# Optimization experiments

Measured on AMD Instinct MI355X. Metric: run time of the kernel, lower is better.

## Reference

```python
import jax, jax.numpy as jnp
import numpy as np

B, S, D = 2, 2048, 2048
VOCAB = 32000
CUTOFFS = [1000, 2000, 5000, VOCAB]  # torch appends vocab_size
N_CLUSTERS = 3
HEAD_SIZE = CUTOFFS[0] + N_CLUSTERS  # 1003
LN_EPS = 1e-5
INIT = 0.02


def setup_inputs() -> dict:
    key = jax.random.key(0)
    ks = jax.random.split(key, 10)
    inp = {
        "x": jax.random.normal(ks[0], (B, S, D), dtype=jnp.float32),
        "targets": jax.random.randint(ks[1], (B, S), 0, VOCAB, dtype=jnp.int32),
        "gamma": jnp.ones((D,), jnp.float32),
        "beta": jnp.zeros((D,), jnp.float32),
        "head_w": jax.random.normal(ks[2], (HEAD_SIZE, D), jnp.float32) * INIT,
    }
    # tail clusters: hsz = D // 4**i, osz = cutoffs[i] - cutoffs[i-1]
    for i in range(1, 4):
        hsz = D // (4 ** i)
        osz = CUTOFFS[i] - CUTOFFS[i - 1]
        inp[f"t{i}_w1"] = jax.random.normal(ks[2 + 2 * i], (hsz, D), jnp.float32) * INIT
        inp[f"t{i}_w2"] = jax.random.normal(ks[3 + 2 * i], (osz, hsz), jnp.float32) * INIT
    return inp


def reference(x, targets, gamma, beta, head_w, t1_w1, t1_w2, t2_w1, t2_w2, t3_w1, t3_w2):
    # LayerNorm over last dim
    mu = jnp.mean(x, axis=-1, keepdims=True)
    var = jnp.mean(jnp.square(x - mu), axis=-1, keepdims=True)
    xn = (x - mu) * jax.lax.rsqrt(var + LN_EPS) * gamma + beta

    # shift: predict token t+1 from hidden t
    h = xn[:, :-1, :].reshape(-1, x.shape[-1])      # [N, D]
    lbl = targets[:, 1:].reshape(-1)                # [N]
    n = h.shape[0]
    rows = jnp.arange(n)

    # head: shortlist (first cutoff) + one logit per tail cluster
    head_lp = jax.nn.log_softmax(h @ head_w.T, axis=-1)  # [N, 1003]
    out = head_lp[rows, jnp.clip(lbl, 0, CUTOFFS[0] - 1)]

    tails = [(t1_w1, t1_w2), (t2_w1, t2_w2), (t3_w1, t3_w2)]
    for i, (w1, w2) in enumerate(tails):
        low, high = CUTOFFS[i], CUTOFFS[i + 1]
        tail_lp = jax.nn.log_softmax((h @ w1.T) @ w2.T, axis=-1)  # [N, osz]
        rel = jnp.clip(lbl - low, 0, high - low - 1)
        lp = head_lp[:, CUTOFFS[0] + i] + tail_lp[rows, rel]
        out = jnp.where((lbl >= low) & (lbl < high), lp, out)

    return -jnp.mean(out)  # NLL loss, matches .loss of AdaptiveLogSoftmaxWithLoss
```

## Files before the change

### kernel.cpp

```cpp
#include <hip/hip_runtime.h>
#include <hip/hip_bf16.h>
#include <math.h>

#define BB 2
#define SS 2048
#define DD 2048
#define NR (BB*(SS-1))
#define NRP 4096
#define MC_LD 1792
#define MT_LD 768
#define MT_P2 512
#define MT_P3 640

#define L2E 1.4426950408889634f
#define LSE_SHIFT 4.0f
#define LSE_NC (-LSE_SHIFT * L2E)
#define WSCALE 16.0f
#define WINV   0.0625f

typedef short  bh8   __attribute__((ext_vector_type(8)));
typedef float  f32x4 __attribute__((ext_vector_type(4)));
typedef long   l64x2 __attribute__((ext_vector_type(2)));

__device__ inline float bfl(unsigned short b) { return __uint_as_float(((unsigned)b) << 16); }
__device__ inline float expsh(float v) { return __builtin_amdgcn_exp2f(fmaf(v, L2E, LSE_NC)); }

__device__ inline float block_sum256(float v) {
    __shared__ float tmp[4];
    #pragma unroll
    for (int o = 32; o > 0; o >>= 1) v += __shfl_down(v, o, 64);
    int lane = threadIdx.x & 63, w = threadIdx.x >> 6;
    if (lane == 0) tmp[w] = v;
    __syncthreads();
    float r = tmp[0] + tmp[1] + tmp[2] + tmp[3];
    __syncthreads();
    return r;
}

__device__ inline unsigned pack_fp8x4(float a, float b, float c, float d) {
    unsigned r = 0;
    r = __builtin_amdgcn_cvt_pk_fp8_f32(a, b, r, false);
    r = __builtin_amdgcn_cvt_pk_fp8_f32(c, d, r, true);
    return r;
}

struct CastSegs {
    const float* src[7];
    void* dst[7];
    int n_src[7];
    int n_tot[7];
    int b0[7];
    int isfp8[7];
};
struct AParams {
    const float* x; const float* gamma; const float* beta;
    unsigned char* h8;
    CastSegs sg; int castBlocks;
    const int* targets;
    int *relH, *rel1, *rel2, *rel3;
    float *S1, *S2, *out;
};

__global__ __launch_bounds__(256) void stageA(AParams p) {
    int blk = blockIdx.x, tid = threadIdx.x;
    if (blk < NRP) {
        int n = blk;
        unsigned char* hr = p.h8 + (size_t)n * DD;
        if (n >= NR) { *(uint2*)(hr + tid * 8) = make_uint2(0,0); return; }
        int b = n / (SS - 1), t = n % (SS - 1);
        const float4* xr = (const float4*)(p.x + (size_t)(b * SS + t) * DD);
        float4 a = xr[tid * 2];
        float4 c = xr[tid * 2 + 1];
        float sum = a.x + a.y + a.z + a.w + c.x + c.y + c.z + c.w;
        sum = block_sum256(sum);
        float mu = sum * (1.0f / DD);
        float d[8] = {a.x-mu, a.y-mu, a.z-mu, a.w-mu, c.x-mu, c.y-mu, c.z-mu, c.w-mu};
        float sq = 0.f;
        #pragma unroll
        for (int i = 0; i < 8; ++i) sq += d[i] * d[i];
        sq = block_sum256(sq);
        float rstd = rsqrtf(sq * (1.0f / DD) + 1e-5f);
        const float4* g4 = (const float4*)p.gamma;
        const float4* be4 = (const float4*)p.beta;
        float4 g1 = g4[tid*2], g2 = g4[tid*2+1];
        float4 b1 = be4[tid*2], b2 = be4[tid*2+1];
        float gg[8] = {g1.x,g1.y,g1.z,g1.w,g2.x,g2.y,g2.z,g2.w};
        float bb[8] = {b1.x,b1.y,b1.z,b1.w,b2.x,b2.y,b2.z,b2.w};
        float o[8];
        #pragma unroll
        for (int i = 0; i < 8; ++i) o[i] = d[i] * rstd * gg[i] + bb[i];
        uint2 pk;
        pk.x = pack_fp8x4(o[0], o[1], o[2], o[3]);
        pk.y = pack_fp8x4(o[4], o[5], o[6], o[7]);
        *(uint2*)(hr + tid * 8) = pk;
        return;
    }
    blk -= NRP;
    if (blk < p.castBlocks) {
        int k = 0;
        #pragma unroll
        for (int i = 1; i < 7; ++i) if (blk >= p.sg.b0[i]) k = i;
        int i4 = (blk - p.sg.b0[k]) * 1024 + tid * 4;
        if (i4 >= p.sg.n_tot[k]) return;
        float4 v = make_float4(0.f,0.f,0.f,0.f);
        if (i4 < p.sg.n_src[k]) v = *(const float4*)(p.sg.src[k] + i4);
        if (p.sg.isfp8[k]) {
            unsigned pk = pack_fp8x4(v.x * WSCALE, v.y * WSCALE, v.z * WSCALE, v.w * WSCALE);
            *(unsigned*)((unsigned char*)p.sg.dst[k] + i4) = pk;
        } else {
            __align__(8) __hip_bfloat16 o[4] = {
                __float2bfloat16(v.x), __float2bfloat16(v.y),
                __float2bfloat16(v.z), __float2bfloat16(v.w)};
            *(uint2*)((__hip_bfloat16*)p.sg.dst[k] + i4) = *(uint2*)o;
        }
        return;
    }
    blk -= p.castBlocks;
    int n = blk * 256 + tid;
    if (n >= NRP) return;
    int lbl = -1;
    if (n < NR) {
        int b = n / (SS - 1), t = n % (SS - 1);
        lbl = p.targets[b * SS + t + 1];
    }
    bool v = n < NR;
    p.relH[n] = v ? (lbl < 1000 ? lbl : 999) : -1;
    int r1 = lbl - 1000;  p.rel1[n] = v ? (r1 < 0 ? 0 : (r1 > 999   ? 999   : r1)) : -1;
    int r2 = lbl - 2000;  p.rel2[n] = v ? (r2 < 0 ? 0 : (r2 > 2999  ? 2999  : r2)) : -1;
    int r3 = lbl - 5000;  p.rel3[n] = v ? (r3 < 0 ? 0 : (r3 > 26999 ? 26999 : r3)) : -1;
    p.S1[n] = 0.f; p.S2[n] = 0.f;
    if (n == 0) p.out[0] = 0.f;
}

__global__ __launch_bounds__(256) void mega_sk(
        const unsigned char* __restrict__ A,
        const unsigned char* __restrict__ W,
        __hip_bfloat16* __restrict__ P) {
    __shared__ __align__(16) unsigned char As[128 * 64];
    __shared__ __align__(16) unsigned char Ws[128 * 64];
    int tid = threadIdx.x, wv = tid >> 6, lane = tid & 63;
    int row0 = blockIdx.y * 128, col0 = blockIdx.x * 128;
    int kb = blockIdx.z * 1024, ke = kb + 1024;
    int wrow = (wv >> 1) * 64, wcol = (wv & 1) * 64;
    f32x4 acc[4][4];
    #pragma unroll
    for (int i = 0; i < 4; ++i)
        #pragma unroll
        for (int j = 0; j < 4; ++j) acc[i][j] = (f32x4){0.f,0.f,0.f,0.f};
    int sr = lane >> 2;
    int kp = (lane & 3) * 16;
    int mrow = lane & 15;
    int q16 = (lane >> 4) * 16;

    for (int k0 = kb; k0 < ke; k0 += 64) {
        __syncthreads();
        #pragma unroll
        for (int i = 0; i < 2; ++i) {
            int chunk = wv * 2 + i;
            int r = chunk * 16 + sr;
            const void* ga = A + (size_t)(row0 + r) * DD + k0 + kp;
            const void* gw = W + (size_t)(col0 + r) * DD + k0 + kp;
            void* la = (char*)As + chunk * 1024 + lane * 16;
            void* lw = (char*)Ws + chunk * 1024 + lane * 16;
            __builtin_amdgcn_global_load_lds(
                (const __attribute__((address_space(1))) void*)ga,
                (__attribute__((address_space(3))) void*)la, 16, 0, 0);
            __builtin_amdgcn_global_load_lds(
                (const __attribute__((address_space(1))) void*)gw,
                (__attribute__((address_space(3))) void*)lw, 16, 0, 0);
        }
        __syncthreads();
        l64x2 af[4], bfr[4];
        #pragma unroll
        for (int t = 0; t < 4; ++t) {
            af[t]  = *(const l64x2*)(As + (wrow + t*16 + mrow) * 64 + q16);
            bfr[t] = *(const l64x2*)(Ws + (wcol + t*16 + mrow) * 64 + q16);
        }
        #pragma unroll
        for (int s = 0; s < 2; ++s)
            #pragma unroll
            for (int i = 0; i < 4; ++i)
                #pragma unroll
                for (int j = 0; j < 4; ++j)
                    acc[i][j] = __builtin_amdgcn_mfma_f32_16x16x32_fp8_fp8(
                        af[i][s], bfr[j][s], acc[i][j], 0, 0, 0);
    }
    __hip_bfloat16* Cz = P + (size_t)blockIdx.z * NRP * MC_LD;
    int ccol = lane & 15, crow = (lane >> 4) * 4;
    #pragma unroll
    for (int i = 0; i < 4; ++i) {
        size_t gr0 = row0 + wrow + i*16 + crow;
        #pragma unroll
        for (int j = 0; j < 4; ++j) {
            size_t gc = col0 + wcol + j*16 + ccol;
            #pragma unroll
            for (int r = 0; r < 4; ++r)
                Cz[(gr0 + r) * MC_LD + gc] = __float2bfloat16(acc[i][j][r] * WINV);
        }
    }
}

__global__ __launch_bounds__(256) void combine_head(
        const __hip_bfloat16* __restrict__ P,
        __hip_bfloat16* __restrict__ megaT,
        const int* __restrict__ relH,
        float* __restrict__ S0, float* __restrict__ aux) {
    int n = blockIdx.x, t = threadIdx.x;
    float s = 0.f;
    if (t < 224) {
        int c0 = t * 8;
        bh8 v0 = *(const bh8*)(P + (size_t)n * MC_LD + c0);
        bh8 v1 = *(const bh8*)(P + (size_t)NRP * MC_LD + (size_t)n * MC_LD + c0);
        float v[8];
        #pragma unroll
        for (int e = 0; e < 8; ++e)
            v[e] = bfl(((unsigned short*)&v0)[e]) + bfl(((unsigned short*)&v1)[e]);
        if (c0 < 1024) {
            int rh = relH[n];
            #pragma unroll
            for (int e = 0; e < 8; ++e) {
                int c = c0 + e;
                if (c < 1003) s += expsh(v[e]);
                if (c == rh) aux[n*8 + 0] = v[e];
                if (c >= 1000 && c < 1003) aux[n*8 + 2 + (c - 1000)] = v[e];
            }
        } else {
            __align__(16) __hip_bfloat16 o[8];
            #pragma unroll
            for (int e = 0; e < 8; ++e) o[e] = __float2bfloat16(v[e]);
            *(uint4*)(megaT + (size_t)n * MT_LD + (c0 - 1024)) = *(uint4*)o;
        }
    }
    s = block_sum256(s);
    if (t == 0) S0[n] = s;
}

__device__ void tail_gemm(const __hip_bfloat16* A, int lda,
        const __hip_bfloat16* W, int K, int bx, int by, int validCols,
        const int* rel, float* S, float* tgt, char* sm) {
    __hip_bfloat16* As = (__hip_bfloat16*)sm;
    __hip_bfloat16* Ws = (__hip_bfloat16*)(sm + 4096);
    int tid = threadIdx.x, wv = tid >> 6, lane = tid & 63;
    int row0 = by * 64, col0 = bx * 128;
    int wrow = (wv >> 1) * 32, wcol = (wv & 1) * 64;
    f32x4 acc[2][4];
    #pragma unroll
    for (int i = 0; i < 2; ++i)
        #pragma unroll
        for (int j = 0; j < 4; ++j) acc[i][j] = (f32x4){0.f,0.f,0.f,0.f};
    int sr = lane >> 2, sk = (lane & 3) * 8, mrow = lane & 15, q16 = (lane >> 4) * 16;

    for (int k0 = 0; k0 < K; k0 += 32) {
        __syncthreads();
        #pragma unroll
        for (int i = 0; i < 3; ++i) {
            int c = wv * 3 + i;
            const __hip_bfloat16* gsrc;
            char* ldst;
            if (c < 4) {
                gsrc = A + (size_t)(row0 + c * 16 + sr) * lda + k0 + sk;
                ldst = (char*)As + c * 1024 + lane * 16;
            } else {
                int cw = c - 4;
                gsrc = W + (size_t)(col0 + cw * 16 + sr) * K + k0 + sk;
                ldst = (char*)Ws + cw * 1024 + lane * 16;
            }
            __builtin_amdgcn_global_load_lds(
                (const __attribute__((address_space(1))) void*)gsrc,
                (__attribute__((address_space(3))) void*)ldst, 16, 0, 0);
        }
        __syncthreads();
        bh8 af[2], bfr[4];
        #pragma unroll
        for (int t = 0; t < 2; ++t)
            af[t] = *(const bh8*)((const char*)As + (wrow + t*16 + mrow) * 64 + q16);
        #pragma unroll
        for (int t = 0; t < 4; ++t)
            bfr[t] = *(const bh8*)((const char*)Ws + (wcol + t*16 + mrow) * 64 + q16);
        #pragma unroll
        for (int i = 0; i < 2; ++i)
            #pragma unroll
            for (int j = 0; j < 4; ++j)
                acc[i][j] = __builtin_amdgcn_mfma_f32_16x16x32_bf16(af[i], bfr[j], acc[i][j], 0, 0, 0);
    }
    int ccol = lane & 15, g = lane >> 4;
    int grs[2][4], rh[2][4];
    float p[2][4];
    #pragma unroll
    for (int i = 0; i < 2; ++i)
        #pragma unroll
        for (int r = 0; r < 4; ++r) {
            grs[i][r] = row0 + wrow + i*16 + g*4 + r;
            rh[i][r] = rel[grs[i][r]];
            p[i][r] = 0.f;
        }
    #pragma unroll
    for (int i = 0; i < 2; ++i)
        #pragma unroll
        for (int j = 0; j < 4; ++j) {
            int gc = col0 + wcol + j*16 + ccol;
            bool inr = gc < validCols;
            #pragma unroll
            for (int r = 0; r < 4; ++r) {
                float v = acc[i][j][r];
                if (gc == rh[i][r]) tgt[grs[i][r]] = v;
                p[i][r] += inr ? expsh(v) : 0.f;
            }
        }
    #pragma unroll
    for (int off = 1; off < 16; off <<= 1)
        #pragma unroll
        for (int i = 0; i < 2; ++i)
            #pragma unroll
            for (int r = 0; r < 4; ++r) p[i][r] += __shfl_xor(p[i][r], off, 64);
    if (ccol == 0)
        #pragma unroll
        for (int i = 0; i < 2; ++i)
            #pragma unroll
            for (int r = 0; r < 4; ++r) atomicAdd(&S[grs[i][r]], p[i][r]);
}

__device__ void t3_partial_body(const __hip_bfloat16* megaT,
        const __hip_bfloat16* w2b, float* pS, int idx, int tid, float* red ) {
    int rg = idx >> 3, cs = idx & 7;
    int wv = tid >> 6, lane = tid & 63;
    int q = lane >> 4, cm = lane & 15;
    int row0 = rg * 32;
    bh8 af0 = *(const bh8*)(megaT + (size_t)(row0 + cm) * MT_LD + MT_P3 + q * 8);
    bh8 af1 = *(const bh8*)(megaT + (size_t)(row0 + 16 + cm) * MT_LD + MT_P3 + q * 8);
    int tile0 = cs * 211, tile1 = tile0 + 211;
    float s0[4] = {0,0,0,0}, s1[4] = {0,0,0,0};
    bh8 bf = *(const bh8*)(w2b + (size_t)((tile0 + wv) * 16 + cm) * 32 + q * 8);
    for (int ot = tile0 + wv; ot < tile1; ot += 4) {
        int otn = ot + 4;
        bh8 bfn = bf;
        if (otn < tile1)
            bfn = *(const bh8*)(w2b + (size_t)(otn * 16 + cm) * 32 + q * 8);
        f32x4 c0 = __builtin_amdgcn_mfma_f32_16x16x32_bf16(af0, bf, (f32x4){0,0,0,0}, 0, 0, 0);
        f32x4 c1 = __builtin_amdgcn_mfma_f32_16x16x32_bf16(af1, bf, (f32x4){0,0,0,0}, 0, 0, 0);
        #pragma unroll
        for (int r = 0; r < 4; ++r) { s0[r] += expsh(c0[r]); s1[r] += expsh(c1[r]); }
        bf = bfn;
    }
    #pragma unroll
    for (int off = 1; off < 16; off <<= 1)
        #pragma unroll
        for (int r = 0; r < 4; ++r) {
            s0[r] += __shfl_xor(s0[r], off, 64);
            s1[r] += __shfl_xor(s1[r], off, 64);
        }
    if (cm == 0)
        #pragma unroll
        for (int r = 0; r < 4; ++r) {
            red[wv * 32 + q * 4 + r]      = s0[r];
            red[wv * 32 + 16 + q * 4 + r] = s1[r];
        }
    __syncthreads();
    if (tid < 32)
        pS[(size_t)(row0 + tid) * 8 + cs] = red[tid] + red[32 + tid] + red[64 + tid] + red[96 + tid];
}

__device__ void t3_gather_body(const __hip_bfloat16* megaT, const __hip_bfloat16* w2b,
        const int* rel3, float* tt2, int idx, int tid) {
    int n = idx * 256 + tid;
    if (n >= NR) return;
    int rc = rel3[n];
    const unsigned short* pa = (const unsigned short*)(megaT + (size_t)n * MT_LD + MT_P3);
    const unsigned short* pw = (const unsigned short*)(w2b + (size_t)rc * 32);
    float acc = 0.f;
    #pragma unroll
    for (int k = 0; k < 32; ++k) acc += bfl(pa[k]) * bfl(pw[k]);
    tt2[n] = acc;
}

#define NT3 1024
#define NT1 512
#define NT2 1536
__global__ __launch_bounds__(256) void fatC(const __hip_bfloat16* __restrict__ megaT,
        const __hip_bfloat16* __restrict__ t1w2b, const __hip_bfloat16* __restrict__ t2w2b,
        const __hip_bfloat16* __restrict__ w2b3,
        const int* __restrict__ rel1, const int* __restrict__ rel2, const int* __restrict__ rel3,
        float* __restrict__ S1, float* __restrict__ S2, float* __restrict__ pS3,
        float* __restrict__ tt0, float* __restrict__ tt1, float* __restrict__ tt2) {
    __shared__ __align__(16) char sm[12288];
    int idx = blockIdx.x, tid = threadIdx.x;
    if (idx < NT3) { t3_partial_body(megaT, w2b3, pS3, idx, tid, (float*)sm); return; }
    idx -= NT3;
    if (idx < NT1) { tail_gemm(megaT, MT_LD, t1w2b, 512, idx % 8, idx / 8, 1000, rel1, S1, tt0, sm); return; }
    idx -= NT1;
    if (idx < NT2) { tail_gemm(megaT + MT_P2, MT_LD, t2w2b, 128, idx % 24, idx / 24, 3000, rel2, S2, tt1, sm); return; }
    idx -= NT2;
    t3_gather_body(megaT, w2b3, rel3, tt2, idx, tid);
}

__global__ __launch_bounds__(256) void final_kernel(const float* __restrict__ aux,
        const int* __restrict__ targets,
        const float* __restrict__ S0, const float* __restrict__ S1, const float* __restrict__ S2,
        const float* __restrict__ pS3,
        const float* __restrict__ tt0, const float* __restrict__ tt1, const float* __restrict__ tt2,
        float* __restrict__ out) {
    int n = blockIdx.x * 256 + threadIdx.x;
    float local = 0.f;
    if (n < NR) {
        int b = n / (SS - 1), t = n % (SS - 1);
        int lbl = targets[b * SS + t + 1];
        float lse = logf(S0[n]) + LSE_SHIFT;
        float o;
        if (lbl < 1000)      o = aux[n*8 + 0] - lse;
        else if (lbl < 2000) o = (aux[n*8 + 2] - lse) + (tt0[n] - (logf(S1[n]) + LSE_SHIFT));
        else if (lbl < 5000) o = (aux[n*8 + 3] - lse) + (tt1[n] - (logf(S2[n]) + LSE_SHIFT));
        else {
            float S3 = 0.f;
            #pragma unroll
            for (int c = 0; c < 8; ++c) S3 += pS3[n*8 + c];
            S3 -= 8.0f * __builtin_amdgcn_exp2f(LSE_NC);
            o = (aux[n*8 + 4] - lse) + (tt2[n] - (logf(S3) + LSE_SHIFT));
        }
        local = o;
    }
    local = block_sum256(local);
    if (threadIdx.x == 0) atomicAdd(out, -local / (float)NR);
}

extern "C" void kernel_launch(void* const* d_in, const int* in_sizes, int n_in,
                              void* d_out, int out_size, void* d_ws, size_t ws_size,
                              hipStream_t stream) {
    const float* x      = (const float*)d_in[0];
    const int*   targets= (const int*)d_in[1];
    const float* gamma  = (const float*)d_in[2];
    const float* beta   = (const float*)d_in[3];
    const float* head_w = (const float*)d_in[4];
    const float* t1_w1  = (const float*)d_in[5];
    const float* t1_w2  = (const float*)d_in[6];
    const float* t2_w1  = (const float*)d_in[7];
    const float* t2_w2  = (const float*)d_in[8];
    const float* t3_w1  = (const float*)d_in[9];
    const float* t3_w2  = (const float*)d_in[10];
    (void)in_sizes; (void)n_in; (void)out_size; (void)ws_size;

    char* base = (char*)d_ws;
    size_t off = 0;
    auto ab = [&](size_t nbytes) { char* p = base + off; off += (nbytes + 15) & ~(size_t)15; return p; };
    unsigned char* h8     = (unsigned char*)ab((size_t)NRP * DD);
    unsigned char* w1cat8 = (unsigned char*)ab((size_t)MC_LD * DD);
    __hip_bfloat16* P     = (__hip_bfloat16*)ab((size_t)2 * NRP * MC_LD * 2);
    __hip_bfloat16* megaT = (__hip_bfloat16*)ab((size_t)NRP * MT_LD * 2);
    __hip_bfloat16* t1w2b = (__hip_bfloat16*)ab((size_t)1024 * 512 * 2);
    __hip_bfloat16* t2w2b = (__hip_bfloat16*)ab((size_t)3072 * 128 * 2);
    __hip_bfloat16* w2b3  = (__hip_bfloat16*)ab((size_t)27008 * 32 * 2);
    float* aux = (float*)ab((size_t)NRP * 8 * 4);
    float* pS3 = (float*)ab((size_t)NRP * 8 * 4);
    float* S0  = (float*)ab(NRP * 4);
    float* S1  = (float*)ab(NRP * 4);
    float* S2  = (float*)ab(NRP * 4);
    int* relH  = (int*)ab(NRP * 4);
    int* rel1  = (int*)ab(NRP * 4);
    int* rel2  = (int*)ab(NRP * 4);
    int* rel3  = (int*)ab(NRP * 4);
    float* tt0 = (float*)ab(NRP * 4);
    float* tt1 = (float*)ab(NRP * 4);
    float* tt2 = (float*)ab(NRP * 4);

    AParams p;
    p.x = x; p.gamma = gamma; p.beta = beta; p.h8 = h8;
    p.targets = targets;
    p.relH = relH; p.rel1 = rel1; p.rel2 = rel2; p.rel3 = rel3;
    p.S1 = S1; p.S2 = S2; p.out = (float*)d_out;
    const float* srcs[7] = {head_w, t1_w1, t2_w1, t3_w1, t1_w2, t2_w2, t3_w2};
    void* dsts[7] = {w1cat8, w1cat8 + (size_t)1024*2048, w1cat8 + (size_t)1536*2048,
                     w1cat8 + (size_t)1664*2048, t1w2b, t2w2b, w2b3};
    int nsrc[7] = {1003*2048, 512*2048, 128*2048, 32*2048, 1000*512, 3000*128, 27000*32};
    int ntot[7] = {1024*2048, 512*2048, 128*2048, 128*2048, 1024*512, 3072*128, 27008*32};
    int isf8[7] = {1, 1, 1, 1, 0, 0, 0};
    int blk = 0;
    for (int i = 0; i < 7; ++i) {
        p.sg.src[i] = srcs[i]; p.sg.dst[i] = dsts[i];
        p.sg.n_src[i] = nsrc[i]; p.sg.n_tot[i] = ntot[i];
        p.sg.isfp8[i] = isf8[i];
        p.sg.b0[i] = blk;
        blk += (ntot[i] + 1023) / 1024;
    }
    p.castBlocks = blk;

    stageA<<<NRP + blk + 16, 256, 0, stream>>>(p);
    mega_sk<<<dim3(14, 32, 2), 256, 0, stream>>>(h8, w1cat8, P);
    combine_head<<<NRP, 256, 0, stream>>>(P, megaT, relH, S0, aux);
    fatC<<<NT3 + NT1 + NT2 + 16, 256, 0, stream>>>(megaT, t1w2b, t2w2b, w2b3,
            rel1, rel2, rel3, S1, S2, pS3, tt0, tt1, tt2);
    final_kernel<<<16, 256, 0, stream>>>(aux, targets, S0, S1, S2, pS3, tt0, tt1, tt2, (float*)d_out);
}
```

Measured before the change: 194.5 us.

## Replace LDS-tiled tail GEMMs with register-resident streaming LSE kernels

Tail clusters 1 and 2 no longer run as LDS-staged 64x128 tiled GEMMs. Each block now keeps its A rows in registers for the whole K, streams W2 column tiles straight from global memory, and accumulates exp sums in registers. Per-row partial sums are reduced through a small shared buffer, leaving one atomic per row instead of many, and the block count for tail 2 drops. Padded zero columns are no longer masked inside the kernel; the final kernel subtracts a constant correction for them, which assumes those padded weight columns are exactly zero.

```diff
diff --git a/kernel.cpp b/kernel.cpp
--- a/kernel.cpp
+++ b/kernel.cpp
@@ -235,89 +235,77 @@
     if (t == 0) S0[n] = s;
 }
 
-__device__ void tail_gemm(const __hip_bfloat16* A, int lda,
-        const __hip_bfloat16* W, int K, int bx, int by, int validCols,
-        const int* rel, float* S, float* tgt, char* sm) {
-    __hip_bfloat16* As = (__hip_bfloat16*)sm;
-    __hip_bfloat16* Ws = (__hip_bfloat16*)(sm + 4096);
+template<int KCH, int ROWS>
+__device__ void stream_lse(const __hip_bfloat16* __restrict__ A, int lda,
+        const __hip_bfloat16* __restrict__ W, int ldw,
+        int rg, int tile0, int ntiles,
+        const int* __restrict__ rel, float* __restrict__ S, float* __restrict__ tgt,
+        float* red) {
+    constexpr int RH = ROWS / 16;
     int tid = threadIdx.x, wv = tid >> 6, lane = tid & 63;
-    int row0 = by * 64, col0 = bx * 128;
-    int wrow = (wv >> 1) * 32, wcol = (wv & 1) * 64;
-    f32x4 acc[2][4];
-    #pragma unroll
-    for (int i = 0; i < 2; ++i)
-        #pragma unroll
-        for (int j = 0; j < 4; ++j) acc[i][j] = (f32x4){0.f,0.f,0.f,0.f};
-    int sr = lane >> 2, sk = (lane & 3) * 8, mrow = lane & 15, q16 = (lane >> 4) * 16;
-
-    for (int k0 = 0; k0 < K; k0 += 32) {
-        __syncthreads();
-        #pragma unroll
-        for (int i = 0; i < 3; ++i) {
-            int c = wv * 3 + i;
-            const __hip_bfloat16* gsrc;
-            char* ldst;
-            if (c < 4) {
-                gsrc = A + (size_t)(row0 + c * 16 + sr) * lda + k0 + sk;
-                ldst = (char*)As + c * 1024 + lane * 16;
-            } else {
-                int cw = c - 4;
-                gsrc = W + (size_t)(col0 + cw * 16 + sr) * K + k0 + sk;
-                ldst = (char*)Ws + cw * 1024 + lane * 16;
+    int q = lane >> 4, cm = lane & 15;
+    int row0 = rg * ROWS;
+    bh8 af[RH][KCH];
+    #pragma unroll
+    for (int h = 0; h < RH; ++h)
+        #pragma unroll
+        for (int c = 0; c < KCH; ++c)
+            af[h][c] = *(const bh8*)(A + (size_t)(row0 + h*16 + cm) * lda + c*32 + q*8);
+    int rc[RH][4];
+    #pragma unroll
+    for (int h = 0; h < RH; ++h)
+        #pragma unroll
+        for (int r = 0; r < 4; ++r)
+            rc[h][r] = rel[row0 + h*16 + q*4 + r];
+    float s[RH][4];
+    #pragma unroll
+    for (int h = 0; h < RH; ++h)
+        #pragma unroll
+        for (int r = 0; r < 4; ++r) s[h][r] = 0.f;
+
+    for (int ot = tile0 + wv; ot < tile0 + ntiles; ot += 4) {
+        const __hip_bfloat16* wr = W + (size_t)(ot*16 + cm) * ldw + q*8;
+        f32x4 acc[RH][2];
+        #pragma unroll
+        for (int h = 0; h < RH; ++h) {
+            acc[h][0] = (f32x4){0.f,0.f,0.f,0.f};
+            acc[h][1] = (f32x4){0.f,0.f,0.f,0.f};
+        }
+        #pragma unroll
+        for (int c = 0; c < KCH; ++c) {
+            bh8 bf = *(const bh8*)(wr + c*32);
+            #pragma unroll
+            for (int h = 0; h < RH; ++h)
+                acc[h][c & 1] = __builtin_amdgcn_mfma_f32_16x16x32_bf16(
+                    af[h][c], bf, acc[h][c & 1], 0, 0, 0);
+        }
+        int gc = ot * 16 + cm;
+        #pragma unroll
+        for (int h = 0; h < RH; ++h)
+            #pragma unroll
+            for (int r = 0; r < 4; ++r) {
+                float v = acc[h][0][r] + acc[h][1][r];
+                if (gc == rc[h][r]) tgt[row0 + h*16 + q*4 + r] = v;
+                s[h][r] += expsh(v);
             }
-            __builtin_amdgcn_global_load_lds(
-                (const __attribute__((address_space(1))) void*)gsrc,
-                (__attribute__((address_space(3))) void*)ldst, 16, 0, 0);
-        }
-        __syncthreads();
-        bh8 af[2], bfr[4];
-        #pragma unroll
-        for (int t = 0; t < 2; ++t)
-            af[t] = *(const bh8*)((const char*)As + (wrow + t*16 + mrow) * 64 + q16);
-        #pragma unroll
-        for (int t = 0; t < 4; ++t)
-            bfr[t] = *(const bh8*)((const char*)Ws + (wcol + t*16 + mrow) * 64 + q16);
-        #pragma unroll
-        for (int i = 0; i < 2; ++i)
-            #pragma unroll
-            for (int j = 0; j < 4; ++j)
-                acc[i][j] = __builtin_amdgcn_mfma_f32_16x16x32_bf16(af[i], bfr[j], acc[i][j], 0, 0, 0);
-    }
-    int ccol = lane & 15, g = lane >> 4;
-    int grs[2][4], rh[2][4];
-    float p[2][4];
-    #pragma unroll
-    for (int i = 0; i < 2; ++i)
-        #pragma unroll
-        for (int r = 0; r < 4; ++r) {
-            grs[i][r] = row0 + wrow + i*16 + g*4 + r;
-            rh[i][r] = rel[grs[i][r]];
-            p[i][r] = 0.f;
-        }
-    #pragma unroll
-    for (int i = 0; i < 2; ++i)
-        #pragma unroll
-        for (int j = 0; j < 4; ++j) {
-            int gc = col0 + wcol + j*16 + ccol;
-            bool inr = gc < validCols;
-            #pragma unroll
-            for (int r = 0; r < 4; ++r) {
-                float v = acc[i][j][r];
-                if (gc == rh[i][r]) tgt[grs[i][r]] = v;
-                p[i][r] += inr ? expsh(v) : 0.f;
-            }
-        }
+    }
     #pragma unroll
     for (int off = 1; off < 16; off <<= 1)
         #pragma unroll
-        for (int i = 0; i < 2; ++i)
-            #pragma unroll
-            for (int r = 0; r < 4; ++r) p[i][r] += __shfl_xor(p[i][r], off, 64);
-    if (ccol == 0)
-        #pragma unroll
-        for (int i = 0; i < 2; ++i)
-            #pragma unroll
-            for (int r = 0; r < 4; ++r) atomicAdd(&S[grs[i][r]], p[i][r]);
+        for (int h = 0; h < RH; ++h)
+            #pragma unroll
+            for (int r = 0; r < 4; ++r)
+                s[h][r] += __shfl_xor(s[h][r], off, 64);
+    if (cm == 0)
+        #pragma unroll
+        for (int h = 0; h < RH; ++h)
+            #pragma unroll
+            for (int r = 0; r < 4; ++r)
+                red[wv * ROWS + h*16 + q*4 + r] = s[h][r];
+    __syncthreads();
+    if (tid < ROWS)
+        atomicAdd(&S[row0 + tid],
+                  red[tid] + red[ROWS + tid] + red[2*ROWS + tid] + red[3*ROWS + tid]);
 }
 
 __device__ void t3_partial_body(const __hip_bfloat16* megaT,
@@ -375,20 +363,28 @@
 
 #define NT3 1024
 #define NT1 512
-#define NT2 1536
+#define NT2 512
 __global__ __launch_bounds__(256) void fatC(const __hip_bfloat16* __restrict__ megaT,
         const __hip_bfloat16* __restrict__ t1w2b, const __hip_bfloat16* __restrict__ t2w2b,
         const __hip_bfloat16* __restrict__ w2b3,
         const int* __restrict__ rel1, const int* __restrict__ rel2, const int* __restrict__ rel3,
         float* __restrict__ S1, float* __restrict__ S2, float* __restrict__ pS3,
         float* __restrict__ tt0, float* __restrict__ tt1, float* __restrict__ tt2) {
-    __shared__ __align__(16) char sm[12288];
+    __shared__ float red[128];
     int idx = blockIdx.x, tid = threadIdx.x;
-    if (idx < NT3) { t3_partial_body(megaT, w2b3, pS3, idx, tid, (float*)sm); return; }
+    if (idx < NT3) { t3_partial_body(megaT, w2b3, pS3, idx, tid, red); return; }
     idx -= NT3;
-    if (idx < NT1) { tail_gemm(megaT, MT_LD, t1w2b, 512, idx % 8, idx / 8, 1000, rel1, S1, tt0, sm); return; }
+    if (idx < NT1) {
+        int rg = idx >> 1, cs = idx & 1;
+        stream_lse<16,16>(megaT, MT_LD, t1w2b, 512, rg, cs * 32, 32, rel1, S1, tt0, red);
+        return;
+    }
     idx -= NT1;
-    if (idx < NT2) { tail_gemm(megaT + MT_P2, MT_LD, t2w2b, 128, idx % 24, idx / 24, 3000, rel2, S2, tt1, sm); return; }
+    if (idx < NT2) {
+        int rg = idx >> 2, cs = idx & 3;
+        stream_lse<4,32>(megaT + MT_P2, MT_LD, t2w2b, 128, rg, cs * 48, 48, rel2, S2, tt1, red);
+        return;
+    }
     idx -= NT2;
     t3_gather_body(megaT, w2b3, rel3, tt2, idx, tid);
 }
@@ -402,18 +398,19 @@
     int n = blockIdx.x * 256 + threadIdx.x;
     float local = 0.f;
     if (n < NR) {
+        float E = __builtin_amdgcn_exp2f(LSE_NC);
         int b = n / (SS - 1), t = n % (SS - 1);
         int lbl = targets[b * SS + t + 1];
         float lse = logf(S0[n]) + LSE_SHIFT;
         float o;
         if (lbl < 1000)      o = aux[n*8 + 0] - lse;
-        else if (lbl < 2000) o = (aux[n*8 + 2] - lse) + (tt0[n] - (logf(S1[n]) + LSE_SHIFT));
-        else if (lbl < 5000) o = (aux[n*8 + 3] - lse) + (tt1[n] - (logf(S2[n]) + LSE_SHIFT));
+        else if (lbl < 2000) o = (aux[n*8 + 2] - lse) + (tt0[n] - (logf(S1[n] - 24.f*E) + LSE_SHIFT));
+        else if (lbl < 5000) o = (aux[n*8 + 3] - lse) + (tt1[n] - (logf(S2[n] - 72.f*E) + LSE_SHIFT));
         else {
             float S3 = 0.f;
             #pragma unroll
             for (int c = 0; c < 8; ++c) S3 += pS3[n*8 + c];
-            S3 -= 8.0f * __builtin_amdgcn_exp2f(LSE_NC);
+            S3 -= 8.0f * E;
             o = (aux[n*8 + 4] - lse) + (tt2[n] - (logf(S3) + LSE_SHIFT));
         }
         local = o;
```

After: 221.4 us. 13.8% more time.

## Drop split-K in head GEMM and fuse head log-sum-exp epilogue

Applied to the files above, without the earlier changes.

Removes the two-way split-K of the fused head/tail-projection GEMM and the separate combine kernel. The GEMM epilogue now computes per-row exp sums with shuffles and atomics into S0, captures target and cluster logits directly, and writes the tail hidden activations to megaT. This drops the large bf16 partial buffer round trip and one launch. In exchange the grid shrinks from 896 to 448 blocks, each doing twice the K loop, which may leave CUs underused on this GPU.

```diff
diff --git a/kernel.cpp b/kernel.cpp
--- a/kernel.cpp
+++ b/kernel.cpp
@@ -7,7 +7,6 @@
 #define DD 2048
 #define NR (BB*(SS-1))
 #define NRP 4096
-#define MC_LD 1792
 #define MT_LD 768
 #define MT_P2 512
 #define MT_P3 640
@@ -58,7 +57,7 @@
     CastSegs sg; int castBlocks;
     const int* targets;
     int *relH, *rel1, *rel2, *rel3;
-    float *S1, *S2, *out;
+    float *S0, *S1, *S2, *out;
 };
 
 __global__ __launch_bounds__(256) void stageA(AParams p) {
@@ -128,19 +127,20 @@
     int r1 = lbl - 1000;  p.rel1[n] = v ? (r1 < 0 ? 0 : (r1 > 999   ? 999   : r1)) : -1;
     int r2 = lbl - 2000;  p.rel2[n] = v ? (r2 < 0 ? 0 : (r2 > 2999  ? 2999  : r2)) : -1;
     int r3 = lbl - 5000;  p.rel3[n] = v ? (r3 < 0 ? 0 : (r3 > 26999 ? 26999 : r3)) : -1;
-    p.S1[n] = 0.f; p.S2[n] = 0.f;
+    p.S0[n] = 0.f; p.S1[n] = 0.f; p.S2[n] = 0.f;
     if (n == 0) p.out[0] = 0.f;
 }
 
-__global__ __launch_bounds__(256) void mega_sk(
+__global__ __launch_bounds__(256) void megaF(
         const unsigned char* __restrict__ A,
         const unsigned char* __restrict__ W,
-        __hip_bfloat16* __restrict__ P) {
+        __hip_bfloat16* __restrict__ megaT,
+        const int* __restrict__ relH,
+        float* __restrict__ S0, float* __restrict__ aux) {
     __shared__ __align__(16) unsigned char As[128 * 64];
     __shared__ __align__(16) unsigned char Ws[128 * 64];
     int tid = threadIdx.x, wv = tid >> 6, lane = tid & 63;
     int row0 = blockIdx.y * 128, col0 = blockIdx.x * 128;
-    int kb = blockIdx.z * 1024, ke = kb + 1024;
     int wrow = (wv >> 1) * 64, wcol = (wv & 1) * 64;
     f32x4 acc[4][4];
     #pragma unroll
@@ -152,7 +152,7 @@
     int mrow = lane & 15;
     int q16 = (lane >> 4) * 16;
 
-    for (int k0 = kb; k0 < ke; k0 += 64) {
+    for (int k0 = 0; k0 < DD; k0 += 64) {
         __syncthreads();
         #pragma unroll
         for (int i = 0; i < 2; ++i) {
@@ -185,54 +185,57 @@
                     acc[i][j] = __builtin_amdgcn_mfma_f32_16x16x32_fp8_fp8(
                         af[i][s], bfr[j][s], acc[i][j], 0, 0, 0);
     }
-    __hip_bfloat16* Cz = P + (size_t)blockIdx.z * NRP * MC_LD;
-    int ccol = lane & 15, crow = (lane >> 4) * 4;
-    #pragma unroll
-    for (int i = 0; i < 4; ++i) {
-        size_t gr0 = row0 + wrow + i*16 + crow;
-        #pragma unroll
-        for (int j = 0; j < 4; ++j) {
-            size_t gc = col0 + wcol + j*16 + ccol;
-            #pragma unroll
-            for (int r = 0; r < 4; ++r)
-                Cz[(gr0 + r) * MC_LD + gc] = __float2bfloat16(acc[i][j][r] * WINV);
-        }
-    }
-}
-
-__global__ __launch_bounds__(256) void combine_head(
-        const __hip_bfloat16* __restrict__ P,
-        __hip_bfloat16* __restrict__ megaT,
-        const int* __restrict__ relH,
-        float* __restrict__ S0, float* __restrict__ aux) {
-    int n = blockIdx.x, t = threadIdx.x;
-    float s = 0.f;
-    if (t < 224) {
-        int c0 = t * 8;
-        bh8 v0 = *(const bh8*)(P + (size_t)n * MC_LD + c0);
-        bh8 v1 = *(const bh8*)(P + (size_t)NRP * MC_LD + (size_t)n * MC_LD + c0);
-        float v[8];
-        #pragma unroll
-        for (int e = 0; e < 8; ++e)
-            v[e] = bfl(((unsigned short*)&v0)[e]) + bfl(((unsigned short*)&v1)[e]);
-        if (c0 < 1024) {
-            int rh = relH[n];
-            #pragma unroll
-            for (int e = 0; e < 8; ++e) {
-                int c = c0 + e;
-                if (c < 1003) s += expsh(v[e]);
-                if (c == rh) aux[n*8 + 0] = v[e];
-                if (c >= 1000 && c < 1003) aux[n*8 + 2 + (c - 1000)] = v[e];
+    int ccol = lane & 15, g = lane >> 4;
+    if (blockIdx.x < 8) {
+        int grs[4][4], rh[4][4];
+        float ps[4][4];
+        #pragma unroll
+        for (int i = 0; i < 4; ++i)
+            #pragma unroll
+            for (int r = 0; r < 4; ++r) {
+                grs[i][r] = row0 + wrow + i*16 + g*4 + r;
+                rh[i][r] = relH[grs[i][r]];
+                ps[i][r] = 0.f;
             }
-        } else {
-            __align__(16) __hip_bfloat16 o[8];
-            #pragma unroll
-            for (int e = 0; e < 8; ++e) o[e] = __float2bfloat16(v[e]);
-            *(uint4*)(megaT + (size_t)n * MT_LD + (c0 - 1024)) = *(uint4*)o;
-        }
-    }
-    s = block_sum256(s);
-    if (t == 0) S0[n] = s;
+        #pragma unroll
+        for (int i = 0; i < 4; ++i)
+            #pragma unroll
+            for (int j = 0; j < 4; ++j) {
+                int gc = col0 + wcol + j*16 + ccol;
+                bool inr = gc < 1003;
+                #pragma unroll
+                for (int r = 0; r < 4; ++r) {
+                    float v = acc[i][j][r] * WINV;
+                    if (gc == rh[i][r]) aux[grs[i][r]*8 + 0] = v;
+                    if (gc >= 1000 && gc < 1003) aux[grs[i][r]*8 + 2 + (gc - 1000)] = v;
+                    ps[i][r] += inr ? expsh(v) : 0.f;
+                }
+            }
+        #pragma unroll
+        for (int off = 1; off < 16; off <<= 1)
+            #pragma unroll
+            for (int i = 0; i < 4; ++i)
+                #pragma unroll
+                for (int r = 0; r < 4; ++r) ps[i][r] += __shfl_xor(ps[i][r], off, 64);
+        if (ccol == 0)
+            #pragma unroll
+            for (int i = 0; i < 4; ++i)
+                #pragma unroll
+                for (int r = 0; r < 4; ++r) atomicAdd(&S0[grs[i][r]], ps[i][r]);
+    } else {
+        int cb = col0 - 1024 + wcol;
+        #pragma unroll
+        for (int i = 0; i < 4; ++i) {
+            size_t gr0 = row0 + wrow + i*16 + g*4;
+            #pragma unroll
+            for (int j = 0; j < 4; ++j) {
+                size_t gc = cb + j*16 + ccol;
+                #pragma unroll
+                for (int r = 0; r < 4; ++r)
+                    megaT[(gr0 + r) * MT_LD + gc] = __float2bfloat16(acc[i][j][r] * WINV);
+            }
+        }
+    }
 }
 
 __device__ void tail_gemm(const __hip_bfloat16* A, int lda,
@@ -442,8 +445,7 @@
     size_t off = 0;
     auto ab = [&](size_t nbytes) { char* p = base + off; off += (nbytes + 15) & ~(size_t)15; return p; };
     unsigned char* h8     = (unsigned char*)ab((size_t)NRP * DD);
-    unsigned char* w1cat8 = (unsigned char*)ab((size_t)MC_LD * DD);
-    __hip_bfloat16* P     = (__hip_bfloat16*)ab((size_t)2 * NRP * MC_LD * 2);
+    unsigned char* w1cat8 = (unsigned char*)ab((size_t)1792 * DD);
     __hip_bfloat16* megaT = (__hip_bfloat16*)ab((size_t)NRP * MT_LD * 2);
     __hip_bfloat16* t1w2b = (__hip_bfloat16*)ab((size_t)1024 * 512 * 2);
     __hip_bfloat16* t2w2b = (__hip_bfloat16*)ab((size_t)3072 * 128 * 2);
@@ -465,7 +467,7 @@
     p.x = x; p.gamma = gamma; p.beta = beta; p.h8 = h8;
     p.targets = targets;
     p.relH = relH; p.rel1 = rel1; p.rel2 = rel2; p.rel3 = rel3;
-    p.S1 = S1; p.S2 = S2; p.out = (float*)d_out;
+    p.S0 = S0; p.S1 = S1; p.S2 = S2; p.out = (float*)d_out;
     const float* srcs[7] = {head_w, t1_w1, t2_w1, t3_w1, t1_w2, t2_w2, t3_w2};
     void* dsts[7] = {w1cat8, w1cat8 + (size_t)1024*2048, w1cat8 + (size_t)1536*2048,
                      w1cat8 + (size_t)1664*2048, t1w2b, t2w2b, w2b3};
@@ -483,8 +485,7 @@
     p.castBlocks = blk;
 
     stageA<<<NRP + blk + 16, 256, 0, stream>>>(p);
-    mega_sk<<<dim3(14, 32, 2), 256, 0, stream>>>(h8, w1cat8, P);
-    combine_head<<<NRP, 256, 0, stream>>>(P, megaT, relH, S0, aux);
+    megaF<<<dim3(14, 32), 256, 0, stream>>>(h8, w1cat8, megaT, relH, S0, aux);
     fatC<<<NT3 + NT1 + NT2 + 16, 256, 0, stream>>>(megaT, t1w2b, t2w2b, w2b3,
             rel1, rel2, rel3, S1, S2, pS3, tt0, tt1, tt2);
     final_kernel<<<16, 256, 0, stream>>>(aux, targets, S0, S1, S2, pS3, tt0, tt1, tt2, (float*)d_out);
```

New measurement: 193.3 us. No clear change (-0.6%).
